# Performance work log

Hardware: AMD Instinct MI355X
Metric: run time of the kernel (lower is better)

## Reference

```python
import jax, jax.numpy as jnp
import numpy as np

P = 100   # num_proxies
N = 1024  # num_samples
D = 512


def _edge_index():
    # complete bipartite proxy<->sample graph, both directions, plus self-loops
    # (PyG GATConv adds self-loops for all nodes by default)
    p = np.arange(P)
    s = np.arange(P, P + N)
    src_ps = np.repeat(p, N)   # proxy -> sample
    dst_ps = np.tile(s, P)
    loops = np.arange(P + N)
    src = np.concatenate([src_ps, dst_ps, loops]).astype(np.int32)
    dst = np.concatenate([dst_ps, src_ps, loops]).astype(np.int32)
    return jnp.asarray(src), jnp.asarray(dst)


def setup_inputs() -> dict:
    key = jax.random.key(0)
    ks = jax.random.split(key, 10)
    sc = 1.0 / np.sqrt(D)
    src, dst = _edge_index()
    return {
        "x": jax.random.normal(ks[0], (N, D), jnp.float32),
        "proxies": jax.random.normal(ks[1], (P, D), jnp.float32),
        "W1": jax.random.normal(ks[2], (D, D), jnp.float32) * sc,
        "a_src1": jax.random.normal(ks[3], (D,), jnp.float32) * sc,
        "a_dst1": jax.random.normal(ks[4], (D,), jnp.float32) * sc,
        "b1": jnp.zeros((D,), jnp.float32),
        "W2": jax.random.normal(ks[5], (D, D), jnp.float32) * sc,
        "a_src2": jax.random.normal(ks[6], (D,), jnp.float32) * sc,
        "a_dst2": jax.random.normal(ks[7], (D,), jnp.float32) * sc,
        "b2": jnp.zeros((D,), jnp.float32),
        "fc_w": jax.random.normal(ks[8], (D, 100), jnp.float32) * sc,
        "fc_b": jnp.zeros((100,), jnp.float32),
        "src": src,
        "dst": dst,
    }


def _gat_conv(x, src, dst, W, a_src, a_dst, b, n_nodes):
    # PyG GATConv, heads=1, concat=True, negative_slope=0.2
    h = x @ W                      # [n, D]
    l_src = h @ a_src              # [n]
    l_dst = h @ a_dst              # [n]
    e = jax.nn.leaky_relu(l_src[src] + l_dst[dst], 0.2)   # [E]
    # segment softmax over edges sharing the same destination
    e = e - jax.ops.segment_max(e, dst, num_segments=n_nodes)[dst]
    ex = jnp.exp(e)
    denom = jax.ops.segment_sum(ex, dst, num_segments=n_nodes)[dst]
    alpha = ex / denom             # [E]
    out = jax.ops.segment_sum(alpha[:, None] * h[src], dst, num_segments=n_nodes)
    return out + b


def reference(x, proxies, W1, a_src1, a_dst1, b1, W2, a_src2, a_dst2, b2, fc_w, fc_b, src, dst):
    n = P + N
    h = jnp.concatenate([proxies, x], axis=0)          # [P+N, D]
    h = jax.nn.relu(_gat_conv(h, src, dst, W1, a_src1, a_dst1, b1, n))
    # Dropout -> identity (eval)
    h = jax.nn.relu(_gat_conv(h, src, dst, W2, a_src2, a_dst2, b2, n))
    preds = h @ fc_w + fc_b                            # [P+N, 100]
    return preds[P:], h[P:]
```

## Files before the change

### kernel.cpp

```cpp
#include <hip/hip_runtime.h>

#define PP 100
#define NS 1024
#define NN 1124
#define DD 512
#define CC 100
#define NTHR 256

typedef _Float16 f16;
typedef _Float16 f16x8 __attribute__((ext_vector_type(8)));
typedef float    f32x4 __attribute__((ext_vector_type(4)));

__device__ __forceinline__ float lk(float v) { return v > 0.f ? v : 0.2f * v; }
__device__ __forceinline__ f16 hif(float v) { return (f16)v; }
__device__ __forceinline__ f16 lof(float v) { return (f16)(v - (float)((f16)v)); }


__device__ __forceinline__ void mgemm_core(
    const f16* __restrict__ Ah, const f16* __restrict__ Al,
    const f16* __restrict__ Bth, const f16* __restrict__ Btl,
    int K, int row0, int col0, f16* __restrict__ lds, f32x4 acc[2][2])
{
  const int t = threadIdx.x;
  const int lane = t & 63, w = t >> 6;
  const int wr = w >> 1, wc = w & 1;
  const int srow = t >> 2, su = t & 3;
  const size_t aoff = (size_t)(row0 + srow) * K + su * 8;
  const size_t boff = (size_t)(col0 + srow) * K + su * 8;
  const int lw = srow * 40 + su * 8;
  const int fra = wr * 32 + (lane & 15);
  const int frb = wc * 32 + (lane & 15);
  const int fu  = (lane >> 4) * 8;
  f32x4 pa0 = *(const f32x4*)(Ah + aoff);
  f32x4 pa1 = *(const f32x4*)(Al + aoff);
  f32x4 pb0 = *(const f32x4*)(Bth + boff);
  f32x4 pb1 = *(const f32x4*)(Btl + boff);
  *(f32x4*)(lds + 0    + lw) = pa0;
  *(f32x4*)(lds + 2560 + lw) = pa1;
  *(f32x4*)(lds + 5120 + lw) = pb0;
  *(f32x4*)(lds + 7680 + lw) = pb1;
  if (K > 32) {
    pa0 = *(const f32x4*)(Ah + aoff + 32);
    pa1 = *(const f32x4*)(Al + aoff + 32);
    pb0 = *(const f32x4*)(Bth + boff + 32);
    pb1 = *(const f32x4*)(Btl + boff + 32);
  }
  __syncthreads();
  int cur = 0;
  for (int kt = 32; kt <= K; kt += 32) {
    f16* rb = lds + cur * 10240;
    f16* wb = lds + (cur ^ 1) * 10240;
    f16x8 ah[2], al[2], bh[2], bl[2];
#pragma unroll
    for (int m = 0; m < 2; ++m) {
      ah[m] = *(const f16x8*)(rb + (fra + m * 16) * 40 + fu);
      al[m] = *(const f16x8*)(rb + 2560 + (fra + m * 16) * 40 + fu);
    }
#pragma unroll
    for (int n = 0; n < 2; ++n) {
      bh[n] = *(const f16x8*)(rb + 5120 + (frb + n * 16) * 40 + fu);
      bl[n] = *(const f16x8*)(rb + 7680 + (frb + n * 16) * 40 + fu);
    }
    if (kt < K) {
      *(f32x4*)(wb + 0    + lw) = pa0;
      *(f32x4*)(wb + 2560 + lw) = pa1;
      *(f32x4*)(wb + 5120 + lw) = pb0;
      *(f32x4*)(wb + 7680 + lw) = pb1;
      if (kt + 32 < K) {
        pa0 = *(const f32x4*)(Ah + aoff + kt + 32);
        pa1 = *(const f32x4*)(Al + aoff + kt + 32);
        pb0 = *(const f32x4*)(Bth + boff + kt + 32);
        pb1 = *(const f32x4*)(Btl + boff + kt + 32);
      }
    }
#pragma unroll
    for (int m = 0; m < 2; ++m)
#pragma unroll
      for (int n = 0; n < 2; ++n) {
        acc[m][n] = __builtin_amdgcn_mfma_f32_16x16x32_f16(ah[m], bh[n], acc[m][n], 0, 0, 0);
        acc[m][n] = __builtin_amdgcn_mfma_f32_16x16x32_f16(al[m], bh[n], acc[m][n], 0, 0, 0);
        acc[m][n] = __builtin_amdgcn_mfma_f32_16x16x32_f16(ah[m], bl[n], acc[m][n], 0, 0, 0);
      }
    __syncthreads();
    cur ^= 1;
  }
}

__device__ __forceinline__ void agg_core(
    const float* __restrict__ lsrc, int kvalid,
    const float* __restrict__ ldb, const float* __restrict__ lsb,
    const f16* __restrict__ Bth, const f16* __restrict__ Btl,
    int K, int row0, int col0, int rvalid,
    const float* __restrict__ selfv,
    f16* __restrict__ outh, f16* __restrict__ outl,
    f16* __restrict__ lds, float* __restrict__ fred)
{
  const int t = threadIdx.x, lane = t & 63, w = t >> 6;
  const int wr = w >> 1, wc = w & 1;
  float* zred = fred;
  float* res  = fred + 256;
  float* riz  = fred + 320;
  const int srow = t >> 2, su = t & 3;
  float sm = -1e30f;
  for (int k = t; k < kvalid; k += NTHR) sm = fmaxf(sm, lsrc[k]);
#pragma unroll
  for (int off = 1; off < 64; off <<= 1) sm = fmaxf(sm, __shfl_xor(sm, off));
  if (lane == 0) zred[w] = sm;
  __syncthreads();
  sm = fmaxf(fmaxf(zred[0], zred[1]), fmaxf(zred[2], zred[3]));
  __syncthreads();
  const bool rok = (row0 + srow) < rvalid;
  float ldr = 0.f, mr = 0.f;
  if (rok) {
    ldr = ldb[row0 + srow];
    mr  = lk(fmaxf(sm, lsb[row0 + srow]) + ldr);
  }
  const size_t boff = (size_t)(col0 + srow) * K + su * 8;
  const int lw = srow * 40 + su * 8;
  const int fra = wr * 32 + (lane & 15);
  const int frb = wc * 32 + (lane & 15);
  const int fu  = (lane >> 4) * 8;
  f32x4 acc[2][2] = {};
  float zacc = 0.f;
  f32x4 pl0 = *(const f32x4*)(lsrc + su * 8);
  f32x4 pl1 = *(const f32x4*)(lsrc + su * 8 + 4);
  f32x4 pb0 = *(const f32x4*)(Bth + boff);
  f32x4 pb1 = *(const f32x4*)(Btl + boff);
  {
    f16x8 ae, al8;
#pragma unroll
    for (int j = 0; j < 8; ++j) {
      const int k = su * 8 + j;
      const float lv = (j < 4) ? pl0[j] : pl1[j - 4];
      float f = 0.f;
      if (rok && k < kvalid) f = __expf(lk(lv + ldr) - mr);
      zacc += f;
      ae[j] = hif(f); al8[j] = lof(f);
    }
    *(f16x8*)(lds + 0    + lw) = ae;
    *(f16x8*)(lds + 2560 + lw) = al8;
    *(f32x4*)(lds + 5120 + lw) = pb0;
    *(f32x4*)(lds + 7680 + lw) = pb1;
  }
  if (K > 32) {
    pl0 = *(const f32x4*)(lsrc + 32 + su * 8);
    pl1 = *(const f32x4*)(lsrc + 32 + su * 8 + 4);
    pb0 = *(const f32x4*)(Bth + boff + 32);
    pb1 = *(const f32x4*)(Btl + boff + 32);
  }
  __syncthreads();
  int cur = 0;
  for (int kt = 32; kt <= K; kt += 32) {
    f16* rb = lds + cur * 10240;
    f16* wb = lds + (cur ^ 1) * 10240;
    f16x8 ah[2], alr[2], bh[2], bl[2];
#pragma unroll
    for (int m = 0; m < 2; ++m) {
      ah[m]  = *(const f16x8*)(rb + (fra + m * 16) * 40 + fu);
      alr[m] = *(const f16x8*)(rb + 2560 + (fra + m * 16) * 40 + fu);
    }
#pragma unroll
    for (int n = 0; n < 2; ++n) {
      bh[n] = *(const f16x8*)(rb + 5120 + (frb + n * 16) * 40 + fu);
      bl[n] = *(const f16x8*)(rb + 7680 + (frb + n * 16) * 40 + fu);
    }
    if (kt < K) {
      f16x8 ae, al8;
      const int k0 = kt + su * 8;
#pragma unroll
      for (int j = 0; j < 8; ++j) {
        const int k = k0 + j;
        const float lv = (j < 4) ? pl0[j] : pl1[j - 4];
        float f = 0.f;
        if (rok && k < kvalid) f = __expf(lk(lv + ldr) - mr);
        zacc += f;
        ae[j] = hif(f); al8[j] = lof(f);
      }
      *(f16x8*)(wb + 0    + lw) = ae;
      *(f16x8*)(wb + 2560 + lw) = al8;
      *(f32x4*)(wb + 5120 + lw) = pb0;
      *(f32x4*)(wb + 7680 + lw) = pb1;
      if (kt + 32 < K) {
        pl0 = *(const f32x4*)(lsrc + kt + 32 + su * 8);
        pl1 = *(const f32x4*)(lsrc + kt + 32 + su * 8 + 4);
        pb0 = *(const f32x4*)(Bth + boff + kt + 32);
        pb1 = *(const f32x4*)(Btl + boff + kt + 32);
      }
    }
#pragma unroll
    for (int m = 0; m < 2; ++m)
#pragma unroll
      for (int n = 0; n < 2; ++n) {
        acc[m][n] = __builtin_amdgcn_mfma_f32_16x16x32_f16(ah[m],  bh[n], acc[m][n], 0, 0, 0);
        acc[m][n] = __builtin_amdgcn_mfma_f32_16x16x32_f16(alr[m], bh[n], acc[m][n], 0, 0, 0);
        acc[m][n] = __builtin_amdgcn_mfma_f32_16x16x32_f16(ah[m],  bl[n], acc[m][n], 0, 0, 0);
      }
    __syncthreads();
    cur ^= 1;
  }
  zred[t] = zacc;
  __syncthreads();
  if (t < 64) {
    float z = zred[t * 4] + zred[t * 4 + 1] + zred[t * 4 + 2] + zred[t * 4 + 3];
    float es = 0.f, iz = 0.f;
    if (row0 + t < rvalid) {
      const float l2 = ldb[row0 + t], s2 = lsb[row0 + t];
      const float m2 = lk(fmaxf(sm, s2) + l2);
      es = __expf(lk(s2 + l2) - m2);
      iz = 1.f / (z + es);
    }
    res[t] = es; riz[t] = iz;
  }
  __syncthreads();
#pragma unroll
  for (int m = 0; m < 2; ++m)
#pragma unroll
    for (int q = 0; q < 4; ++q) {
      const int rl = wr * 32 + m * 16 + (lane >> 4) * 4 + q;
      const int gr = row0 + rl;
      if (gr >= rvalid) continue;
      const float es = res[rl], iz = riz[rl];
#pragma unroll
      for (int n = 0; n < 2; ++n) {
        const int c = col0 + wc * 32 + n * 16 + (lane & 15);
        const float v = (acc[m][n][q] + es * selfv[(size_t)gr * DD + c]) * iz;
        outh[(size_t)gr * DD + c] = hif(v);
        outl[(size_t)gr * DD + c] = lof(v);
      }
    }
}

__device__ __forceinline__ void cvt_tile(
    const float* __restrict__ in, int R, int Cin,
    f16* __restrict__ oh, f16* __restrict__ ol, int ldo,
    int ti, int tj)
{
  const int t = threadIdx.x;
  const int gj0 = tj * 64 + (t & 31) * 2;
  const int i8  = (t >> 5) * 8;
  const bool c0 = gj0 < Cin, c1 = (gj0 + 1) < Cin;
  f16x8 vh0, vl0, vh1, vl1;
#pragma unroll
  for (int e = 0; e < 8; ++e) {
    const int gi = ti * 64 + i8 + e;
    float a = 0.f, b = 0.f;
    if (gi < R) {
      if (c0 && c1) {
        const float2 v = *(const float2*)(in + (size_t)gi * Cin + gj0);
        a = v.x; b = v.y;
      } else if (c0) {
        a = in[(size_t)gi * Cin + gj0];
      }
    }
    vh0[e] = hif(a); vl0[e] = lof(a);
    vh1[e] = hif(b); vl1[e] = lof(b);
  }
  const size_t o0 = (size_t)gj0 * ldo + ti * 64 + i8;
  *(f16x8*)(oh + o0) = vh0;
  *(f16x8*)(ol + o0) = vl0;
  const size_t o1 = o0 + ldo;
  *(f16x8*)(oh + o1) = vh1;
  *(f16x8*)(ol + o1) = vl1;
}

__global__ __launch_bounds__(NTHR) void prep1_k(
    const float* __restrict__ W1, const float* __restrict__ W2,
    const float* __restrict__ as1, const float* __restrict__ ad1,
    const float* __restrict__ as2, const float* __restrict__ ad2,
    float* __restrict__ v1s, float* __restrict__ v1d,
    float* __restrict__ v2s, float* __restrict__ v2d,
    float* __restrict__ ls2, float* __restrict__ ld2,
    float* __restrict__ M1pf, float* __restrict__ zP)
{
  const int u = blockIdx.x;
  if (u < 256) {
    const int wid  = u * 4 + (threadIdx.x >> 6);
    const int lane = threadIdx.x & 63;
    const int r = wid & 511;
    const bool l1 = (wid < 512);
    const float* W = l1 ? W1 : W2;
    const float4* a4 = (const float4*)(l1 ? as1 : as2);
    const float4* b4 = (const float4*)(l1 ? ad1 : ad2);
    const float4* w4 = (const float4*)(W + (size_t)r * DD);
    float4 w0 = w4[lane], w1 = w4[lane + 64];
    float4 a0 = a4[lane], a1 = a4[lane + 64];
    float4 b0 = b4[lane], b1 = b4[lane + 64];
    float s1 = w0.x * a0.x + w0.y * a0.y + w0.z * a0.z + w0.w * a0.w
             + w1.x * a1.x + w1.y * a1.y + w1.z * a1.z + w1.w * a1.w;
    float s2 = w0.x * b0.x + w0.y * b0.y + w0.z * b0.z + w0.w * b0.w
             + w1.x * b1.x + w1.y * b1.y + w1.z * b1.z + w1.w * b1.w;
#pragma unroll
    for (int off = 32; off > 0; off >>= 1) {
      s1 += __shfl_down(s1, off);
      s2 += __shfl_down(s2, off);
    }
    if (lane == 0) {
      (l1 ? v1s : v2s)[r] = s1;
      (l1 ? v1d : v2d)[r] = s2;
    }
  } else if (u == 256) {
    for (int i = threadIdx.x; i < 1152; i += NTHR) { ls2[i] = 0.f; ld2[i] = 0.f; }
    if (threadIdx.x < 128) zP[threadIdx.x] = 0.f;
  } else {
    float4* p4 = (float4*)M1pf + (size_t)(u - 257) * 800;
#pragma unroll
    for (int p = 0; p < 4; ++p) {
      const int i = threadIdx.x + p * 256;
      if (i < 800) p4[i] = make_float4(0.f, 0.f, 0.f, 0.f);
    }
  }
}

__global__ __launch_bounds__(NTHR) void prep2_k(
    const float* __restrict__ x, const float* __restrict__ prox,
    const float* __restrict__ W1, const float* __restrict__ W2,
    const float* __restrict__ fcw,
    const float* __restrict__ v1s, const float* __restrict__ v1d,
    f16* xth, f16* xtl, f16* pth, f16* ptl,
    f16* W1th, f16* W1tl, f16* W2th, f16* W2tl, f16* fwth, f16* fwtl,
    float* __restrict__ ls1, float* __restrict__ ld1)
{
  const int b = blockIdx.x;
  if (b < 64) {
    cvt_tile(W1, 512, 512, W1th, W1tl, 512, b >> 3, b & 7);
  } else if (b < 128) {
    cvt_tile(W2, 512, 512, W2th, W2tl, 512, (b - 64) >> 3, (b - 64) & 7);
  } else if (b < 256) {
    cvt_tile(x, NS, 512, xth, xtl, NS, (b - 128) >> 3, (b - 128) & 7);
  } else if (b < 272) {
    cvt_tile(prox, PP, 512, pth, ptl, 128, (b - 256) >> 3, (b - 256) & 7);
  } else if (b < 288) {
    cvt_tile(fcw, 512, CC, fwth, fwtl, 512, (b - 272) >> 1, (b - 272) & 1);
  } else {
    const int r    = (b - 288) * 4 + (threadIdx.x >> 6);
    const int lane = threadIdx.x & 63;
    if (r >= NN) return;
    const float* row = (r < PP) ? prox + (size_t)r * DD
                                : x + (size_t)(r - PP) * DD;
    const float4* r4 = (const float4*)row;
    const float4* s4 = (const float4*)v1s;
    const float4* d4 = (const float4*)v1d;
    float4 v0 = r4[lane], v1 = r4[lane + 64];
    float4 a0 = s4[lane], a1 = s4[lane + 64];
    float4 b0 = d4[lane], b1 = d4[lane + 64];
    float s1 = v0.x * a0.x + v0.y * a0.y + v0.z * a0.z + v0.w * a0.w
             + v1.x * a1.x + v1.y * a1.y + v1.z * a1.z + v1.w * a1.w;
    float s2 = v0.x * b0.x + v0.y * b0.y + v0.z * b0.z + v0.w * b0.w
             + v1.x * b1.x + v1.y * b1.y + v1.z * b1.z + v1.w * b1.w;
#pragma unroll
    for (int off = 32; off > 0; off >>= 1) {
      s1 += __shfl_down(s1, off);
      s2 += __shfl_down(s2, off);
    }
    if (lane == 0) { ls1[r] = s1; ld1[r] = s2; }
  }
}

__global__ __launch_bounds__(NTHR) void agg1x_k(
    const float* __restrict__ ls1, const float* __restrict__ ld1,
    const f16* __restrict__ pth, const f16* __restrict__ ptl,
    const f16* __restrict__ xth, const f16* __restrict__ xtl,
    const float* __restrict__ x,
    float* __restrict__ M1pf, float* __restrict__ zP,
    f16* __restrict__ M1h, f16* __restrict__ M1l)
{
  __shared__ __align__(16) f16 lds[20480];
  __shared__ float fred[384];
  const int b = blockIdx.x;
  if (b < 128) {
    const int row0 = (b >> 3) * 64, col0 = (b & 7) * 64;
    agg_core(ls1, PP, ld1 + PP, ls1 + PP, pth, ptl, 128, row0, col0, NS,
             x, M1h + (size_t)PP * DD, M1l + (size_t)PP * DD, lds, fred);
    return;
  }
  const int t = threadIdx.x, lane = t & 63, w = t >> 6;
  const int wr = w >> 1, wc = w & 1;
  const int b2 = b - 128;
  const int tile = b2 >> 2, chunk = b2 & 3;
  const int row0 = (tile >> 3) * 64, col0 = (tile & 7) * 64;
  const int k0 = chunk * 256;
  const float* lsrc = ls1 + PP;
  float sm = -1e30f;
  for (int k = t; k < NS; k += NTHR) sm = fmaxf(sm, lsrc[k]);
#pragma unroll
  for (int off = 1; off < 64; off <<= 1) sm = fmaxf(sm, __shfl_xor(sm, off));
  if (lane == 0) fred[w] = sm;
  __syncthreads();
  sm = fmaxf(fmaxf(fred[0], fred[1]), fmaxf(fred[2], fred[3]));
  __syncthreads();
  const int srow = t >> 2, su = t & 3;
  const bool rok = (row0 + srow) < PP;
  float ldr = 0.f, mr = 0.f;
  if (rok) {
    ldr = ld1[row0 + srow];
    mr  = lk(fmaxf(sm, ls1[row0 + srow]) + ldr);
  }
  const size_t boff = (size_t)(col0 + srow) * NS + k0 + su * 8;
  const int lw = srow * 40 + su * 8;
  const int fra = wr * 32 + (lane & 15);
  const int frb = wc * 32 + (lane & 15);
  const int fu  = (lane >> 4) * 8;
  f32x4 acc[2][2] = {};
  float zacc = 0.f;
  f32x4 pl0 = *(const f32x4*)(lsrc + k0 + su * 8);
  f32x4 pl1 = *(const f32x4*)(lsrc + k0 + su * 8 + 4);
  f32x4 pb0 = *(const f32x4*)(xth + boff);
  f32x4 pb1 = *(const f32x4*)(xtl + boff);
  {
    f16x8 ae, al8;
#pragma unroll
    for (int j = 0; j < 8; ++j) {
      const float lv = (j < 4) ? pl0[j] : pl1[j - 4];
      float f = 0.f;
      if (rok) f = __expf(lk(lv + ldr) - mr);
      zacc += f;
      ae[j] = hif(f); al8[j] = lof(f);
    }
    *(f16x8*)(lds + 0    + lw) = ae;
    *(f16x8*)(lds + 2560 + lw) = al8;
    *(f32x4*)(lds + 5120 + lw) = pb0;
    *(f32x4*)(lds + 7680 + lw) = pb1;
  }
  pl0 = *(const f32x4*)(lsrc + k0 + 32 + su * 8);
  pl1 = *(const f32x4*)(lsrc + k0 + 32 + su * 8 + 4);
  pb0 = *(const f32x4*)(xth + boff + 32);
  pb1 = *(const f32x4*)(xtl + boff + 32);
  __syncthreads();
  int cur = 0;
  for (int kt = 32; kt <= 256; kt += 32) {
    f16* rb = lds + cur * 10240;
    f16* wb = lds + (cur ^ 1) * 10240;
    f16x8 ah[2], alr[2], bh[2], bl[2];
#pragma unroll
    for (int m = 0; m < 2; ++m) {
      ah[m]  = *(const f16x8*)(rb + (fra + m * 16) * 40 + fu);
      alr[m] = *(const f16x8*)(rb + 2560 + (fra + m * 16) * 40 + fu);
    }
#pragma unroll
    for (int n = 0; n < 2; ++n) {
      bh[n] = *(const f16x8*)(rb + 5120 + (frb + n * 16) * 40 + fu);
      bl[n] = *(const f16x8*)(rb + 7680 + (frb + n * 16) * 40 + fu);
    }
    if (kt < 256) {
      f16x8 ae, al8;
#pragma unroll
      for (int j = 0; j < 8; ++j) {
        const float lv = (j < 4) ? pl0[j] : pl1[j - 4];
        float f = 0.f;
        if (rok) f = __expf(lk(lv + ldr) - mr);
        zacc += f;
        ae[j] = hif(f); al8[j] = lof(f);
      }
      *(f16x8*)(wb + 0    + lw) = ae;
      *(f16x8*)(wb + 2560 + lw) = al8;
      *(f32x4*)(wb + 5120 + lw) = pb0;
      *(f32x4*)(wb + 7680 + lw) = pb1;
      if (kt + 32 < 256) {
        pl0 = *(const f32x4*)(lsrc + k0 + kt + 32 + su * 8);
        pl1 = *(const f32x4*)(lsrc + k0 + kt + 32 + su * 8 + 4);
        pb0 = *(const f32x4*)(xth + boff + kt + 32);
        pb1 = *(const f32x4*)(xtl + boff + kt + 32);
      }
    }
#pragma unroll
    for (int m = 0; m < 2; ++m)
#pragma unroll
      for (int n = 0; n < 2; ++n) {
        acc[m][n] = __builtin_amdgcn_mfma_f32_16x16x32_f16(ah[m],  bh[n], acc[m][n], 0, 0, 0);
        acc[m][n] = __builtin_amdgcn_mfma_f32_16x16x32_f16(alr[m], bh[n], acc[m][n], 0, 0, 0);
        acc[m][n] = __builtin_amdgcn_mfma_f32_16x16x32_f16(ah[m],  bl[n], acc[m][n], 0, 0, 0);
      }
    __syncthreads();
    cur ^= 1;
  }
  if (col0 == 0) {
    fred[t] = zacc;
    __syncthreads();
    if (t < 64) {
      const int r = row0 + t;
      if (r < PP) {
        float z = fred[t * 4] + fred[t * 4 + 1] + fred[t * 4 + 2] + fred[t * 4 + 3];
        atomicAdd(&zP[r], z);
      }
    }
  }
#pragma unroll
  for (int m = 0; m < 2; ++m)
#pragma unroll
    for (int q = 0; q < 4; ++q) {
      const int gr = row0 + wr * 32 + m * 16 + (lane >> 4) * 4 + q;
      if (gr >= PP) continue;
#pragma unroll
      for (int n = 0; n < 2; ++n) {
        const int c = col0 + wc * 32 + n * 16 + (lane & 15);
        atomicAdd(&M1pf[(size_t)gr * DD + c], acc[m][n][q]);
      }
    }
}

__global__ __launch_bounds__(NTHR) void h1_k(
    const f16* __restrict__ M1h, const f16* __restrict__ M1l,
    const float* __restrict__ M1pf, const float* __restrict__ zP,
    const float* __restrict__ ls1, const float* __restrict__ ld1,
    const float* __restrict__ prox,
    const f16* __restrict__ W1th, const f16* __restrict__ W1tl,
    const float* __restrict__ b1,
    const float* __restrict__ v2s, const float* __restrict__ v2d,
    float* __restrict__ h1, f16* __restrict__ h1pth, f16* __restrict__ h1ptl,
    float* __restrict__ ls2, float* __restrict__ ld2)
{
  __shared__ __align__(16) f16 lds[20480];
  __shared__ float fred[384];
  float* esA = fred + 256;
  float* izA = fred + 320;
  const int t = threadIdx.x, lane = t & 63, w = t >> 6, wr = w >> 1, wc = w & 1;
  const int b = blockIdx.x;
  const int row0 = (b >> 3) * 64, col0 = (b & 7) * 64;
  const bool hasP = (row0 < 128);
  if (hasP) {
    float sm = -1e30f;
    for (int k = t; k < NS; k += NTHR) sm = fmaxf(sm, ls1[PP + k]);
#pragma unroll
    for (int off = 1; off < 64; off <<= 1) sm = fmaxf(sm, __shfl_xor(sm, off));
    if (lane == 0) fred[w] = sm;
    __syncthreads();
    sm = fmaxf(fmaxf(fred[0], fred[1]), fmaxf(fred[2], fred[3]));
    if (t < 64) {
      const int r = row0 + t;
      float es = 0.f, iz = 0.f;
      if (r < PP) {
        const float ldr = ld1[r];
        const float m = lk(fmaxf(sm, ls1[r]) + ldr);
        es = __expf(lk(ls1[r] + ldr) - m);
        iz = 1.f / (zP[r] + es);
      }
      esA[t] = es; izA[t] = iz;
    }
    __syncthreads();
  }
  const int srow = t >> 2, su = t & 3;
  const int ar = row0 + srow;
  const bool isP = ar < PP;
  const size_t aoff = (size_t)ar * DD + su * 8;
  const size_t boff = (size_t)(col0 + srow) * DD + su * 8;
  const int lw = srow * 40 + su * 8;
  const int fra = wr * 32 + (lane & 15);
  const int frb = wc * 32 + (lane & 15);
  const int fu  = (lane >> 4) * 8;
  const float esr = isP ? esA[srow] : 0.f;
  const float izr = isP ? izA[srow] : 0.f;
  f32x4 qa0, qa1, qb0, qb1, pb0, pb1;
  auto loadA = [&](int k) {
    if (isP) {
      qa0 = *(const f32x4*)(M1pf + aoff + k);
      qa1 = *(const f32x4*)(M1pf + aoff + k + 4);
      qb0 = *(const f32x4*)(prox + aoff + k);
      qb1 = *(const f32x4*)(prox + aoff + k + 4);
    } else {
      qa0 = *(const f32x4*)(M1h + aoff + k);
      qa1 = *(const f32x4*)(M1l + aoff + k);
    }
  };
  auto storeA = [&](f16* wb) {
    if (isP) {
      f16x8 hh, ll;
#pragma unroll
      for (int j = 0; j < 8; ++j) {
        const float pv = (j < 4) ? qa0[j] : qa1[j - 4];
        const float xv = (j < 4) ? qb0[j] : qb1[j - 4];
        const float v = (pv + esr * xv) * izr;
        hh[j] = hif(v); ll[j] = lof(v);
      }
      *(f16x8*)(wb + lw) = hh;
      *(f16x8*)(wb + 2560 + lw) = ll;
    } else {
      *(f32x4*)(wb + lw) = qa0;
      *(f32x4*)(wb + 2560 + lw) = qa1;
    }
  };
  f32x4 acc[2][2] = {};
  loadA(0);
  pb0 = *(const f32x4*)(W1th + boff);
  pb1 = *(const f32x4*)(W1tl + boff);
  storeA(lds);
  *(f32x4*)(lds + 5120 + lw) = pb0;
  *(f32x4*)(lds + 7680 + lw) = pb1;
  loadA(32);
  pb0 = *(const f32x4*)(W1th + boff + 32);
  pb1 = *(const f32x4*)(W1tl + boff + 32);
  __syncthreads();
  int cur = 0;
  for (int kt = 32; kt <= DD; kt += 32) {
    f16* rb = lds + cur * 10240;
    f16* wb = lds + (cur ^ 1) * 10240;
    f16x8 ah[2], al[2], bh[2], bl[2];
#pragma unroll
    for (int m = 0; m < 2; ++m) {
      ah[m] = *(const f16x8*)(rb + (fra + m * 16) * 40 + fu);
      al[m] = *(const f16x8*)(rb + 2560 + (fra + m * 16) * 40 + fu);
    }
#pragma unroll
    for (int n = 0; n < 2; ++n) {
      bh[n] = *(const f16x8*)(rb + 5120 + (frb + n * 16) * 40 + fu);
      bl[n] = *(const f16x8*)(rb + 7680 + (frb + n * 16) * 40 + fu);
    }
    if (kt < DD) {
      storeA(wb);
      *(f32x4*)(wb + 5120 + lw) = pb0;
      *(f32x4*)(wb + 7680 + lw) = pb1;
      if (kt + 32 < DD) {
        loadA(kt + 32);
        pb0 = *(const f32x4*)(W1th + boff + kt + 32);
        pb1 = *(const f32x4*)(W1tl + boff + kt + 32);
      }
    }
#pragma unroll
    for (int m = 0; m < 2; ++m)
#pragma unroll
      for (int n = 0; n < 2; ++n) {
        acc[m][n] = __builtin_amdgcn_mfma_f32_16x16x32_f16(ah[m], bh[n], acc[m][n], 0, 0, 0);
        acc[m][n] = __builtin_amdgcn_mfma_f32_16x16x32_f16(al[m], bh[n], acc[m][n], 0, 0, 0);
        acc[m][n] = __builtin_amdgcn_mfma_f32_16x16x32_f16(ah[m], bl[n], acc[m][n], 0, 0, 0);
      }
    __syncthreads();
    cur ^= 1;
  }
  const int c0 = col0 + wc * 32 + (lane & 15);
  const int c1 = c0 + 16;
  const float vs0 = v2s[c0], vs1 = v2s[c1];
  const float vd0 = v2d[c0], vd1 = v2d[c1];
  const float bb0 = b1[c0],  bb1 = b1[c1];
#pragma unroll
  for (int m = 0; m < 2; ++m)
#pragma unroll
    for (int q = 0; q < 4; ++q) {
      const int r = row0 + wr * 32 + m * 16 + (lane >> 4) * 4 + q;
      if (r >= NN) continue;
      float ps = 0.f, pd = 0.f;
#pragma unroll
      for (int n = 0; n < 2; ++n) {
        const int c = (n == 0) ? c0 : c1;
        const float v = fmaxf(acc[m][n][q] + (n == 0 ? bb0 : bb1), 0.f);
        h1[(size_t)r * DD + c] = v;
        ps += v * (n == 0 ? vs0 : vs1);
        pd += v * (n == 0 ? vd0 : vd1);
        if (r < 128) {
          const size_t o = (size_t)c * 128 + r;
          f16 hh = (f16)0.f, ll = (f16)0.f;
          if (r < PP) { hh = hif(v); ll = lof(v); }
          h1pth[o] = hh; h1ptl[o] = ll;
        }
      }
#pragma unroll
      for (int off = 1; off < 16; off <<= 1) {
        ps += __shfl_xor(ps, off);
        pd += __shfl_xor(pd, off);
      }
      if ((lane & 15) == 0) {
        atomicAdd(&ls2[r], ps);
        atomicAdd(&ld2[r], pd);
      }
    }
}

__global__ __launch_bounds__(NTHR) void agg2x_k(
    const float* __restrict__ ls2, const float* __restrict__ ld2,
    const f16* __restrict__ h1pth, const f16* __restrict__ h1ptl,
    const float* __restrict__ h1,
    f16* __restrict__ M2h, f16* __restrict__ M2l)
{
  __shared__ __align__(16) f16 lds[20480];
  __shared__ float fred[384];
  const int b = blockIdx.x;
  const int row0 = (b >> 3) * 64, col0 = (b & 7) * 64;
  agg_core(ls2, PP, ld2 + PP, ls2 + PP, h1pth, h1ptl, 128, row0, col0, NS,
           h1 + (size_t)PP * DD, M2h, M2l, lds, fred);
}

__global__ __launch_bounds__(NTHR) void h2_k(
    const f16* __restrict__ M2h, const f16* __restrict__ M2l,
    const f16* __restrict__ W2th, const f16* __restrict__ W2tl,
    const float* __restrict__ b2, float* __restrict__ h2s,
    f16* __restrict__ h2h, f16* __restrict__ h2l)
{
  __shared__ __align__(16) f16 lds[20480];
  f32x4 acc[2][2] = {};
  const int t = threadIdx.x, lane = t & 63, w = t >> 6, wr = w >> 1, wc = w & 1;
  const int b = blockIdx.x;
  const int row0 = (b >> 3) * 64, col0 = (b & 7) * 64;
  mgemm_core(M2h, M2l, W2th, W2tl, DD, row0, col0, lds, acc);
#pragma unroll
  for (int m = 0; m < 2; ++m)
#pragma unroll
    for (int q = 0; q < 4; ++q) {
      const int r = row0 + wr * 32 + m * 16 + (lane >> 4) * 4 + q;
#pragma unroll
      for (int n = 0; n < 2; ++n) {
        const int c = col0 + wc * 32 + n * 16 + (lane & 15);
        const float v = fmaxf(acc[m][n][q] + b2[c], 0.f);
        const size_t o = (size_t)r * DD + c;
        h2s[o] = v;
        h2h[o] = hif(v); h2l[o] = lof(v);
      }
    }
}

__global__ __launch_bounds__(NTHR) void fc_k(
    const f16* __restrict__ h2h, const f16* __restrict__ h2l,
    const f16* __restrict__ fwth, const f16* __restrict__ fwtl,
    const float* __restrict__ fcb, float* __restrict__ out)
{
  __shared__ __align__(16) f16 lds[20480];
  f32x4 acc[2][2] = {};
  const int t = threadIdx.x, lane = t & 63, w = t >> 6, wr = w >> 1, wc = w & 1;
  const int b = blockIdx.x;
  const int row0 = (b >> 1) * 64, col0 = (b & 1) * 64;
  mgemm_core(h2h, h2l, fwth, fwtl, DD, row0, col0, lds, acc);
#pragma unroll
  for (int m = 0; m < 2; ++m)
#pragma unroll
    for (int q = 0; q < 4; ++q) {
      const int r = row0 + wr * 32 + m * 16 + (lane >> 4) * 4 + q;
#pragma unroll
      for (int n = 0; n < 2; ++n) {
        const int c = col0 + wc * 32 + n * 16 + (lane & 15);
        if (c < CC) out[(size_t)r * CC + c] = acc[m][n][q] + fcb[c];
      }
    }
}

extern "C" void kernel_launch(void* const* d_in, const int* in_sizes, int n_in,
                              void* d_out, int out_size, void* d_ws, size_t ws_size,
                              hipStream_t stream)
{
  const float* x    = (const float*)d_in[0];
  const float* prox = (const float*)d_in[1];
  const float* W1   = (const float*)d_in[2];
  const float* as1  = (const float*)d_in[3];
  const float* ad1  = (const float*)d_in[4];
  const float* b1   = (const float*)d_in[5];
  const float* W2   = (const float*)d_in[6];
  const float* as2  = (const float*)d_in[7];
  const float* ad2  = (const float*)d_in[8];
  const float* b2   = (const float*)d_in[9];
  const float* fcw  = (const float*)d_in[10];
  const float* fcb  = (const float*)d_in[11];
  float* out = (float*)d_out;

  float* F = (float*)d_ws;
  float* h1   = F; F += (size_t)NN * DD;
  float* ls1  = F; F += 1152;
  float* ld1  = F; F += 1152;
  float* ls2  = F; F += 1152;
  float* ld2  = F; F += 1152;
  float* v1s  = F; F += DD;
  float* v1d  = F; F += DD;
  float* v2s  = F; F += DD;
  float* v2d  = F; F += DD;
  float* M1pf = F; F += (size_t)128 * DD;
  float* zP   = F; F += 128;
  f16* H = (f16*)F;
  f16* M1h  = H; H += (size_t)1152 * DD;
  f16* M1l  = H; H += (size_t)1152 * DD;
  f16* M2h  = H; H += (size_t)NS * DD;
  f16* M2l  = H; H += (size_t)NS * DD;
  f16* xth  = H; H += (size_t)DD * NS;
  f16* xtl  = H; H += (size_t)DD * NS;
  f16* pth  = H; H += (size_t)DD * 128;
  f16* ptl  = H; H += (size_t)DD * 128;
  f16* W1th = H; H += (size_t)DD * DD;
  f16* W1tl = H; H += (size_t)DD * DD;
  f16* W2th = H; H += (size_t)DD * DD;
  f16* W2tl = H; H += (size_t)DD * DD;
  f16* fwth = H; H += (size_t)128 * DD;
  f16* fwtl = H; H += (size_t)128 * DD;
  f16* h2h  = H; H += (size_t)NS * DD;
  f16* h2l  = H; H += (size_t)NS * DD;
  f16* h1pth = H; H += (size_t)DD * 128;
  f16* h1ptl = H; H += (size_t)DD * 128;
  float* h2s = out + (size_t)NS * CC;

  dim3 blk(NTHR);
  prep1_k<<<dim3(273), blk, 0, stream>>>(W1, W2, as1, ad1, as2, ad2,
                                         v1s, v1d, v2s, v2d, ls2, ld2,
                                         M1pf, zP);
  prep2_k<<<dim3(569), blk, 0, stream>>>(x, prox, W1, W2, fcw, v1s, v1d,
      xth, xtl, pth, ptl, W1th, W1tl, W2th, W2tl, fwth, fwtl, ls1, ld1);
  agg1x_k<<<dim3(192), blk, 0, stream>>>(ls1, ld1, pth, ptl, xth, xtl,
                                         x, M1pf, zP, M1h, M1l);
  h1_k<<<dim3(144), blk, 0, stream>>>(M1h, M1l, M1pf, zP, ls1, ld1, prox,
                                      W1th, W1tl, b1, v2s, v2d,
                                      h1, h1pth, h1ptl, ls2, ld2);
  agg2x_k<<<dim3(128), blk, 0, stream>>>(ls2, ld2, h1pth, h1ptl, h1, M2h, M2l);
  h2_k<<<dim3(128), blk, 0, stream>>>(M2h, M2l, W2th, W2tl, b2, h2s, h2h, h2l);
  fc_k<<<dim3(32), blk, 0, stream>>>(h2h, h2l, fwth, fwtl, fcb, out);
}
```

Before: 141.9 us.

## Double threads per GEMM block with split A/B loaders and smaller per-wave tiles

Raises GEMM-style kernels from 256 to 512 threads (8 waves), each wave computing a 16x32 subtile instead of 32x32. Loading is split so the first half of the threads stage A (including softmax weight computation) and the second half stage B. This is meant to raise per-block wave parallelism and latency hiding for these small-grid kernels. In exchange each wave reuses its fragments less and issues more LDS fragment reads per MFMA, and the larger blocks may lower occupancy.

```diff
diff --git a/kernel.cpp b/kernel.cpp
--- a/kernel.cpp
+++ b/kernel.cpp
@@ -6,6 +6,7 @@
 #define DD 512
 #define CC 100
 #define NTHR 256
+#define GT  512
 
 typedef _Float16 f16;
 typedef _Float16 f16x8 __attribute__((ext_vector_type(8)));
@@ -15,72 +16,61 @@
 __device__ __forceinline__ f16 hif(float v) { return (f16)v; }
 __device__ __forceinline__ f16 lof(float v) { return (f16)(v - (float)((f16)v)); }
 
+#define MFMA16(a, b, c) __builtin_amdgcn_mfma_f32_16x16x32_f16(a, b, c, 0, 0, 0)
+
 
 __device__ __forceinline__ void mgemm_core(
     const f16* __restrict__ Ah, const f16* __restrict__ Al,
     const f16* __restrict__ Bth, const f16* __restrict__ Btl,
-    int K, int row0, int col0, f16* __restrict__ lds, f32x4 acc[2][2])
+    int K, int row0, int col0, f16* __restrict__ lds, f32x4 acc[2])
 {
   const int t = threadIdx.x;
   const int lane = t & 63, w = t >> 6;
   const int wr = w >> 1, wc = w & 1;
-  const int srow = t >> 2, su = t & 3;
-  const size_t aoff = (size_t)(row0 + srow) * K + su * 8;
-  const size_t boff = (size_t)(col0 + srow) * K + su * 8;
+  const bool isA = t < 256;
+  const int tt = t & 255;
+  const int srow = tt >> 2, su = tt & 3;
   const int lw = srow * 40 + su * 8;
-  const int fra = wr * 32 + (lane & 15);
+  const int sec0 = isA ? 0 : 5120, sec1 = isA ? 2560 : 7680;
+  const f16* g0 = isA ? Ah : Bth;
+  const f16* g1 = isA ? Al : Btl;
+  const size_t goff = (size_t)((isA ? row0 : col0) + srow) * K + su * 8;
+  const int fra = wr * 16 + (lane & 15);
   const int frb = wc * 32 + (lane & 15);
   const int fu  = (lane >> 4) * 8;
-  f32x4 pa0 = *(const f32x4*)(Ah + aoff);
-  f32x4 pa1 = *(const f32x4*)(Al + aoff);
-  f32x4 pb0 = *(const f32x4*)(Bth + boff);
-  f32x4 pb1 = *(const f32x4*)(Btl + boff);
-  *(f32x4*)(lds + 0    + lw) = pa0;
-  *(f32x4*)(lds + 2560 + lw) = pa1;
-  *(f32x4*)(lds + 5120 + lw) = pb0;
-  *(f32x4*)(lds + 7680 + lw) = pb1;
+  f32x4 p0 = *(const f32x4*)(g0 + goff);
+  f32x4 p1 = *(const f32x4*)(g1 + goff);
+  *(f32x4*)(lds + sec0 + lw) = p0;
+  *(f32x4*)(lds + sec1 + lw) = p1;
   if (K > 32) {
-    pa0 = *(const f32x4*)(Ah + aoff + 32);
-    pa1 = *(const f32x4*)(Al + aoff + 32);
-    pb0 = *(const f32x4*)(Bth + boff + 32);
-    pb1 = *(const f32x4*)(Btl + boff + 32);
+    p0 = *(const f32x4*)(g0 + goff + 32);
+    p1 = *(const f32x4*)(g1 + goff + 32);
   }
   __syncthreads();
   int cur = 0;
   for (int kt = 32; kt <= K; kt += 32) {
     f16* rb = lds + cur * 10240;
     f16* wb = lds + (cur ^ 1) * 10240;
-    f16x8 ah[2], al[2], bh[2], bl[2];
-#pragma unroll
-    for (int m = 0; m < 2; ++m) {
-      ah[m] = *(const f16x8*)(rb + (fra + m * 16) * 40 + fu);
-      al[m] = *(const f16x8*)(rb + 2560 + (fra + m * 16) * 40 + fu);
-    }
-#pragma unroll
-    for (int n = 0; n < 2; ++n) {
-      bh[n] = *(const f16x8*)(rb + 5120 + (frb + n * 16) * 40 + fu);
-      bl[n] = *(const f16x8*)(rb + 7680 + (frb + n * 16) * 40 + fu);
-    }
+    f16x8 ah  = *(const f16x8*)(rb + fra * 40 + fu);
+    f16x8 al  = *(const f16x8*)(rb + 2560 + fra * 40 + fu);
+    f16x8 bh0 = *(const f16x8*)(rb + 5120 + frb * 40 + fu);
+    f16x8 bl0 = *(const f16x8*)(rb + 7680 + frb * 40 + fu);
+    f16x8 bh1 = *(const f16x8*)(rb + 5120 + (frb + 16) * 40 + fu);
+    f16x8 bl1 = *(const f16x8*)(rb + 7680 + (frb + 16) * 40 + fu);
     if (kt < K) {
-      *(f32x4*)(wb + 0    + lw) = pa0;
-      *(f32x4*)(wb + 2560 + lw) = pa1;
-      *(f32x4*)(wb + 5120 + lw) = pb0;
-      *(f32x4*)(wb + 7680 + lw) = pb1;
+      *(f32x4*)(wb + sec0 + lw) = p0;
+      *(f32x4*)(wb + sec1 + lw) = p1;
       if (kt + 32 < K) {
-        pa0 = *(const f32x4*)(Ah + aoff + kt + 32);
-        pa1 = *(const f32x4*)(Al + aoff + kt + 32);
-        pb0 = *(const f32x4*)(Bth + boff + kt + 32);
-        pb1 = *(const f32x4*)(Btl + boff + kt + 32);
-      }
-    }
-#pragma unroll
-    for (int m = 0; m < 2; ++m)
-#pragma unroll
-      for (int n = 0; n < 2; ++n) {
-        acc[m][n] = __builtin_amdgcn_mfma_f32_16x16x32_f16(ah[m], bh[n], acc[m][n], 0, 0, 0);
-        acc[m][n] = __builtin_amdgcn_mfma_f32_16x16x32_f16(al[m], bh[n], acc[m][n], 0, 0, 0);
-        acc[m][n] = __builtin_amdgcn_mfma_f32_16x16x32_f16(ah[m], bl[n], acc[m][n], 0, 0, 0);
-      }
+        p0 = *(const f32x4*)(g0 + goff + kt + 32);
+        p1 = *(const f32x4*)(g1 + goff + kt + 32);
+      }
+    }
+    acc[0] = MFMA16(ah, bh0, acc[0]);
+    acc[0] = MFMA16(al, bh0, acc[0]);
+    acc[0] = MFMA16(ah, bl0, acc[0]);
+    acc[1] = MFMA16(ah, bh1, acc[1]);
+    acc[1] = MFMA16(al, bh1, acc[1]);
+    acc[1] = MFMA16(ah, bl1, acc[1]);
     __syncthreads();
     cur ^= 1;
   }
@@ -100,105 +90,94 @@
   float* zred = fred;
   float* res  = fred + 256;
   float* riz  = fred + 320;
-  const int srow = t >> 2, su = t & 3;
   float sm = -1e30f;
-  for (int k = t; k < kvalid; k += NTHR) sm = fmaxf(sm, lsrc[k]);
+  for (int k = t; k < kvalid; k += GT) sm = fmaxf(sm, lsrc[k]);
 #pragma unroll
   for (int off = 1; off < 64; off <<= 1) sm = fmaxf(sm, __shfl_xor(sm, off));
   if (lane == 0) zred[w] = sm;
   __syncthreads();
-  sm = fmaxf(fmaxf(zred[0], zred[1]), fmaxf(zred[2], zred[3]));
-  __syncthreads();
-  const bool rok = (row0 + srow) < rvalid;
-  float ldr = 0.f, mr = 0.f;
-  if (rok) {
+  sm = fmaxf(fmaxf(fmaxf(zred[0], zred[1]), fmaxf(zred[2], zred[3])),
+             fmaxf(fmaxf(zred[4], zred[5]), fmaxf(zred[6], zred[7])));
+  __syncthreads();
+  const bool isA = t < 256;
+  const int tt = t & 255;
+  const int srow = tt >> 2, su = tt & 3;
+  const int lw = srow * 40 + su * 8;
+  bool rok = false; float ldr = 0.f, mr = 0.f;
+  if (isA && (row0 + srow) < rvalid) {
+    rok = true;
     ldr = ldb[row0 + srow];
     mr  = lk(fmaxf(sm, lsb[row0 + srow]) + ldr);
   }
   const size_t boff = (size_t)(col0 + srow) * K + su * 8;
-  const int lw = srow * 40 + su * 8;
-  const int fra = wr * 32 + (lane & 15);
+  const int fra = wr * 16 + (lane & 15);
   const int frb = wc * 32 + (lane & 15);
   const int fu  = (lane >> 4) * 8;
-  f32x4 acc[2][2] = {};
+  f32x4 acc[2] = {};
   float zacc = 0.f;
-  f32x4 pl0 = *(const f32x4*)(lsrc + su * 8);
-  f32x4 pl1 = *(const f32x4*)(lsrc + su * 8 + 4);
-  f32x4 pb0 = *(const f32x4*)(Bth + boff);
-  f32x4 pb1 = *(const f32x4*)(Btl + boff);
-  {
-    f16x8 ae, al8;
-#pragma unroll
-    for (int j = 0; j < 8; ++j) {
-      const int k = su * 8 + j;
-      const float lv = (j < 4) ? pl0[j] : pl1[j - 4];
-      float f = 0.f;
-      if (rok && k < kvalid) f = __expf(lk(lv + ldr) - mr);
-      zacc += f;
-      ae[j] = hif(f); al8[j] = lof(f);
-    }
-    *(f16x8*)(lds + 0    + lw) = ae;
-    *(f16x8*)(lds + 2560 + lw) = al8;
-    *(f32x4*)(lds + 5120 + lw) = pb0;
-    *(f32x4*)(lds + 7680 + lw) = pb1;
-  }
-  if (K > 32) {
-    pl0 = *(const f32x4*)(lsrc + 32 + su * 8);
-    pl1 = *(const f32x4*)(lsrc + 32 + su * 8 + 4);
-    pb0 = *(const f32x4*)(Bth + boff + 32);
-    pb1 = *(const f32x4*)(Btl + boff + 32);
-  }
+  f32x4 p0, p1;
+  if (isA) {
+    p0 = *(const f32x4*)(lsrc + su * 8);
+    p1 = *(const f32x4*)(lsrc + su * 8 + 4);
+  } else {
+    p0 = *(const f32x4*)(Bth + boff);
+    p1 = *(const f32x4*)(Btl + boff);
+  }
+  auto stage = [&](f16* buf, int kbase) {
+    if (isA) {
+      f16x8 ae, al8;
+#pragma unroll
+      for (int j = 0; j < 8; ++j) {
+        const int k = kbase + su * 8 + j;
+        const float lv = (j < 4) ? p0[j] : p1[j - 4];
+        float f = 0.f;
+        if (rok && k < kvalid) f = __expf(lk(lv + ldr) - mr);
+        zacc += f;
+        ae[j] = hif(f); al8[j] = lof(f);
+      }
+      *(f16x8*)(buf + lw) = ae;
+      *(f16x8*)(buf + 2560 + lw) = al8;
+    } else {
+      *(f32x4*)(buf + 5120 + lw) = p0;
+      *(f32x4*)(buf + 7680 + lw) = p1;
+    }
+  };
+  auto prefetch = [&](int k) {
+    if (isA) {
+      p0 = *(const f32x4*)(lsrc + k + su * 8);
+      p1 = *(const f32x4*)(lsrc + k + su * 8 + 4);
+    } else {
+      p0 = *(const f32x4*)(Bth + boff + k);
+      p1 = *(const f32x4*)(Btl + boff + k);
+    }
+  };
+  stage(lds, 0);
+  if (K > 32) prefetch(32);
   __syncthreads();
   int cur = 0;
   for (int kt = 32; kt <= K; kt += 32) {
     f16* rb = lds + cur * 10240;
     f16* wb = lds + (cur ^ 1) * 10240;
-    f16x8 ah[2], alr[2], bh[2], bl[2];
-#pragma unroll
-    for (int m = 0; m < 2; ++m) {
-      ah[m]  = *(const f16x8*)(rb + (fra + m * 16) * 40 + fu);
-      alr[m] = *(const f16x8*)(rb + 2560 + (fra + m * 16) * 40 + fu);
-    }
-#pragma unroll
-    for (int n = 0; n < 2; ++n) {
-      bh[n] = *(const f16x8*)(rb + 5120 + (frb + n * 16) * 40 + fu);
-      bl[n] = *(const f16x8*)(rb + 7680 + (frb + n * 16) * 40 + fu);
-    }
+    f16x8 ah  = *(const f16x8*)(rb + fra * 40 + fu);
+    f16x8 al  = *(const f16x8*)(rb + 2560 + fra * 40 + fu);
+    f16x8 bh0 = *(const f16x8*)(rb + 5120 + frb * 40 + fu);
+    f16x8 bl0 = *(const f16x8*)(rb + 7680 + frb * 40 + fu);
+    f16x8 bh1 = *(const f16x8*)(rb + 5120 + (frb + 16) * 40 + fu);
+    f16x8 bl1 = *(const f16x8*)(rb + 7680 + (frb + 16) * 40 + fu);
     if (kt < K) {
-      f16x8 ae, al8;
-      const int k0 = kt + su * 8;
-#pragma unroll
-      for (int j = 0; j < 8; ++j) {
-        const int k = k0 + j;
-        const float lv = (j < 4) ? pl0[j] : pl1[j - 4];
-        float f = 0.f;
-        if (rok && k < kvalid) f = __expf(lk(lv + ldr) - mr);
-        zacc += f;
-        ae[j] = hif(f); al8[j] = lof(f);
-      }
-      *(f16x8*)(wb + 0    + lw) = ae;
-      *(f16x8*)(wb + 2560 + lw) = al8;
-      *(f32x4*)(wb + 5120 + lw) = pb0;
-      *(f32x4*)(wb + 7680 + lw) = pb1;
-      if (kt + 32 < K) {
-        pl0 = *(const f32x4*)(lsrc + kt + 32 + su * 8);
-        pl1 = *(const f32x4*)(lsrc + kt + 32 + su * 8 + 4);
-        pb0 = *(const f32x4*)(Bth + boff + kt + 32);
-        pb1 = *(const f32x4*)(Btl + boff + kt + 32);
-      }
-    }
-#pragma unroll
-    for (int m = 0; m < 2; ++m)
-#pragma unroll
-      for (int n = 0; n < 2; ++n) {
-        acc[m][n] = __builtin_amdgcn_mfma_f32_16x16x32_f16(ah[m],  bh[n], acc[m][n], 0, 0, 0);
-        acc[m][n] = __builtin_amdgcn_mfma_f32_16x16x32_f16(alr[m], bh[n], acc[m][n], 0, 0, 0);
-        acc[m][n] = __builtin_amdgcn_mfma_f32_16x16x32_f16(ah[m],  bl[n], acc[m][n], 0, 0, 0);
-      }
+      stage(wb, kt);
+      if (kt + 32 < K) prefetch(kt + 32);
+    }
+    acc[0] = MFMA16(ah, bh0, acc[0]);
+    acc[0] = MFMA16(al, bh0, acc[0]);
+    acc[0] = MFMA16(ah, bl0, acc[0]);
+    acc[1] = MFMA16(ah, bh1, acc[1]);
+    acc[1] = MFMA16(al, bh1, acc[1]);
+    acc[1] = MFMA16(ah, bl1, acc[1]);
     __syncthreads();
     cur ^= 1;
   }
-  zred[t] = zacc;
+  if (t < 256) zred[t] = zacc;
   __syncthreads();
   if (t < 64) {
     float z = zred[t * 4] + zred[t * 4 + 1] + zred[t * 4 + 2] + zred[t * 4 + 3];
@@ -213,21 +192,19 @@
   }
   __syncthreads();
 #pragma unroll
-  for (int m = 0; m < 2; ++m)
-#pragma unroll
-    for (int q = 0; q < 4; ++q) {
-      const int rl = wr * 32 + m * 16 + (lane >> 4) * 4 + q;
-      const int gr = row0 + rl;
-      if (gr >= rvalid) continue;
-      const float es = res[rl], iz = riz[rl];
-#pragma unroll
-      for (int n = 0; n < 2; ++n) {
-        const int c = col0 + wc * 32 + n * 16 + (lane & 15);
-        const float v = (acc[m][n][q] + es * selfv[(size_t)gr * DD + c]) * iz;
-        outh[(size_t)gr * DD + c] = hif(v);
-        outl[(size_t)gr * DD + c] = lof(v);
-      }
-    }
+  for (int q = 0; q < 4; ++q) {
+    const int rl = wr * 16 + (lane >> 4) * 4 + q;
+    const int gr = row0 + rl;
+    if (gr >= rvalid) continue;
+    const float es = res[rl], iz = riz[rl];
+#pragma unroll
+    for (int n = 0; n < 2; ++n) {
+      const int c = col0 + wc * 32 + n * 16 + (lane & 15);
+      const float v = (acc[n][q] + es * selfv[(size_t)gr * DD + c]) * iz;
+      outh[(size_t)gr * DD + c] = hif(v);
+      outl[(size_t)gr * DD + c] = lof(v);
+    }
+  }
 }
 
 __device__ __forceinline__ void cvt_tile(
@@ -356,7 +333,7 @@
   }
 }
 
-__global__ __launch_bounds__(NTHR) void agg1x_k(
+__global__ __launch_bounds__(GT) void agg1x_k(
     const float* __restrict__ ls1, const float* __restrict__ ld1,
     const f16* __restrict__ pth, const f16* __restrict__ ptl,
     const f16* __restrict__ xth, const f16* __restrict__ xtl,
@@ -381,100 +358,87 @@
   const int k0 = chunk * 256;
   const float* lsrc = ls1 + PP;
   float sm = -1e30f;
-  for (int k = t; k < NS; k += NTHR) sm = fmaxf(sm, lsrc[k]);
+  for (int k = t; k < NS; k += GT) sm = fmaxf(sm, lsrc[k]);
 #pragma unroll
   for (int off = 1; off < 64; off <<= 1) sm = fmaxf(sm, __shfl_xor(sm, off));
   if (lane == 0) fred[w] = sm;
   __syncthreads();
-  sm = fmaxf(fmaxf(fred[0], fred[1]), fmaxf(fred[2], fred[3]));
-  __syncthreads();
-  const int srow = t >> 2, su = t & 3;
-  const bool rok = (row0 + srow) < PP;
-  float ldr = 0.f, mr = 0.f;
-  if (rok) {
+  sm = fmaxf(fmaxf(fmaxf(fred[0], fred[1]), fmaxf(fred[2], fred[3])),
+             fmaxf(fmaxf(fred[4], fred[5]), fmaxf(fred[6], fred[7])));
+  __syncthreads();
+  const bool isA = t < 256;
+  const int tt = t & 255;
+  const int srow = tt >> 2, su = tt & 3;
+  const int lw = srow * 40 + su * 8;
+  bool rok = false; float ldr = 0.f, mr = 0.f;
+  if (isA && (row0 + srow) < PP) {
+    rok = true;
     ldr = ld1[row0 + srow];
     mr  = lk(fmaxf(sm, ls1[row0 + srow]) + ldr);
   }
   const size_t boff = (size_t)(col0 + srow) * NS + k0 + su * 8;
-  const int lw = srow * 40 + su * 8;
-  const int fra = wr * 32 + (lane & 15);
+  const int fra = wr * 16 + (lane & 15);
   const int frb = wc * 32 + (lane & 15);
   const int fu  = (lane >> 4) * 8;
-  f32x4 acc[2][2] = {};
+  f32x4 acc[2] = {};
   float zacc = 0.f;
-  f32x4 pl0 = *(const f32x4*)(lsrc + k0 + su * 8);
-  f32x4 pl1 = *(const f32x4*)(lsrc + k0 + su * 8 + 4);
-  f32x4 pb0 = *(const f32x4*)(xth + boff);
-  f32x4 pb1 = *(const f32x4*)(xtl + boff);
-  {
-    f16x8 ae, al8;
-#pragma unroll
-    for (int j = 0; j < 8; ++j) {
-      const float lv = (j < 4) ? pl0[j] : pl1[j - 4];
-      float f = 0.f;
-      if (rok) f = __expf(lk(lv + ldr) - mr);
-      zacc += f;
-      ae[j] = hif(f); al8[j] = lof(f);
-    }
-    *(f16x8*)(lds + 0    + lw) = ae;
-    *(f16x8*)(lds + 2560 + lw) = al8;
-    *(f32x4*)(lds + 5120 + lw) = pb0;
-    *(f32x4*)(lds + 7680 + lw) = pb1;
-  }
-  pl0 = *(const f32x4*)(lsrc + k0 + 32 + su * 8);
-  pl1 = *(const f32x4*)(lsrc + k0 + 32 + su * 8 + 4);
-  pb0 = *(const f32x4*)(xth + boff + 32);
-  pb1 = *(const f32x4*)(xtl + boff + 32);
+  f32x4 p0, p1;
+  auto prefetch = [&](int k) {
+    if (isA) {
+      p0 = *(const f32x4*)(lsrc + k0 + k + su * 8);
+      p1 = *(const f32x4*)(lsrc + k0 + k + su * 8 + 4);
+    } else {
+      p0 = *(const f32x4*)(xth + boff + k);
+      p1 = *(const f32x4*)(xtl + boff + k);
+    }
+  };
+  auto stage = [&](f16* buf) {
+    if (isA) {
+      f16x8 ae, al8;
+#pragma unroll
+      for (int j = 0; j < 8; ++j) {
+        const float lv = (j < 4) ? p0[j] : p1[j - 4];
+        float f = 0.f;
+        if (rok) f = __expf(lk(lv + ldr) - mr);
+        zacc += f;
+        ae[j] = hif(f); al8[j] = lof(f);
+      }
+      *(f16x8*)(buf + lw) = ae;
+      *(f16x8*)(buf + 2560 + lw) = al8;
+    } else {
+      *(f32x4*)(buf + 5120 + lw) = p0;
+      *(f32x4*)(buf + 7680 + lw) = p1;
+    }
+  };
+  prefetch(0);
+  stage(lds);
+  prefetch(32);
   __syncthreads();
   int cur = 0;
   for (int kt = 32; kt <= 256; kt += 32) {
     f16* rb = lds + cur * 10240;
     f16* wb = lds + (cur ^ 1) * 10240;
-    f16x8 ah[2], alr[2], bh[2], bl[2];
-#pragma unroll
-    for (int m = 0; m < 2; ++m) {
-      ah[m]  = *(const f16x8*)(rb + (fra + m * 16) * 40 + fu);
-      alr[m] = *(const f16x8*)(rb + 2560 + (fra + m * 16) * 40 + fu);
-    }
-#pragma unroll
-    for (int n = 0; n < 2; ++n) {
-      bh[n] = *(const f16x8*)(rb + 5120 + (frb + n * 16) * 40 + fu);
-      bl[n] = *(const f16x8*)(rb + 7680 + (frb + n * 16) * 40 + fu);
-    }
+    f16x8 ah  = *(const f16x8*)(rb + fra * 40 + fu);
+    f16x8 al  = *(const f16x8*)(rb + 2560 + fra * 40 + fu);
+    f16x8 bh0 = *(const f16x8*)(rb + 5120 + frb * 40 + fu);
+    f16x8 bl0 = *(const f16x8*)(rb + 7680 + frb * 40 + fu);
+    f16x8 bh1 = *(const f16x8*)(rb + 5120 + (frb + 16) * 40 + fu);
+    f16x8 bl1 = *(const f16x8*)(rb + 7680 + (frb + 16) * 40 + fu);
     if (kt < 256) {
-      f16x8 ae, al8;
-#pragma unroll
-      for (int j = 0; j < 8; ++j) {
-        const float lv = (j < 4) ? pl0[j] : pl1[j - 4];
-        float f = 0.f;
-        if (rok) f = __expf(lk(lv + ldr) - mr);
-        zacc += f;
-        ae[j] = hif(f); al8[j] = lof(f);
-      }
-      *(f16x8*)(wb + 0    + lw) = ae;
-      *(f16x8*)(wb + 2560 + lw) = al8;
-      *(f32x4*)(wb + 5120 + lw) = pb0;
-      *(f32x4*)(wb + 7680 + lw) = pb1;
-      if (kt + 32 < 256) {
-        pl0 = *(const f32x4*)(lsrc + k0 + kt + 32 + su * 8);
-        pl1 = *(const f32x4*)(lsrc + k0 + kt + 32 + su * 8 + 4);
-        pb0 = *(const f32x4*)(xth + boff + kt + 32);
-        pb1 = *(const f32x4*)(xtl + boff + kt + 32);
-      }
-    }
-#pragma unroll
-    for (int m = 0; m < 2; ++m)
-#pragma unroll
-      for (int n = 0; n < 2; ++n) {
-        acc[m][n] = __builtin_amdgcn_mfma_f32_16x16x32_f16(ah[m],  bh[n], acc[m][n], 0, 0, 0);
-        acc[m][n] = __builtin_amdgcn_mfma_f32_16x16x32_f16(alr[m], bh[n], acc[m][n], 0, 0, 0);
-        acc[m][n] = __builtin_amdgcn_mfma_f32_16x16x32_f16(ah[m],  bl[n], acc[m][n], 0, 0, 0);
-      }
+      stage(wb);
+      if (kt + 32 < 256) prefetch(kt + 32);
+    }
+    acc[0] = MFMA16(ah, bh0, acc[0]);
+    acc[0] = MFMA16(al, bh0, acc[0]);
+    acc[0] = MFMA16(ah, bl0, acc[0]);
+    acc[1] = MFMA16(ah, bh1, acc[1]);
+    acc[1] = MFMA16(al, bh1, acc[1]);
+    acc[1] = MFMA16(ah, bl1, acc[1]);
     __syncthreads();
     cur ^= 1;
   }
   if (col0 == 0) {
-    fred[t] = zacc;
+    if (t < 256) fred[t] = zacc;
     __syncthreads();
     if (t < 64) {
       const int r = row0 + t;
@@ -485,20 +449,18 @@
     }
   }
 #pragma unroll
-  for (int m = 0; m < 2; ++m)
-#pragma unroll
-    for (int q = 0; q < 4; ++q) {
-      const int gr = row0 + wr * 32 + m * 16 + (lane >> 4) * 4 + q;
-      if (gr >= PP) continue;
-#pragma unroll
-      for (int n = 0; n < 2; ++n) {
-        const int c = col0 + wc * 32 + n * 16 + (lane & 15);
-        atomicAdd(&M1pf[(size_t)gr * DD + c], acc[m][n][q]);
-      }
-    }
-}
-
-__global__ __launch_bounds__(NTHR) void h1_k(
+  for (int q = 0; q < 4; ++q) {
+    const int gr = row0 + wr * 16 + (lane >> 4) * 4 + q;
+    if (gr >= PP) continue;
+#pragma unroll
+    for (int n = 0; n < 2; ++n) {
+      const int c = col0 + wc * 32 + n * 16 + (lane & 15);
+      atomicAdd(&M1pf[(size_t)gr * DD + c], acc[n][q]);
+    }
+  }
+}
+
+__global__ __launch_bounds__(GT) void h1_k(
     const f16* __restrict__ M1h, const f16* __restrict__ M1l,
     const float* __restrict__ M1pf, const float* __restrict__ zP,
     const float* __restrict__ ls1, const float* __restrict__ ld1,
@@ -513,18 +475,20 @@
   __shared__ float fred[384];
   float* esA = fred + 256;
   float* izA = fred + 320;
-  const int t = threadIdx.x, lane = t & 63, w = t >> 6, wr = w >> 1, wc = w & 1;
+  const int t = threadIdx.x, lane = t & 63, w = t >> 6;
+  const int wr = w >> 1, wc = w & 1;
   const int b = blockIdx.x;
   const int row0 = (b >> 3) * 64, col0 = (b & 7) * 64;
   const bool hasP = (row0 < 128);
   if (hasP) {
     float sm = -1e30f;
-    for (int k = t; k < NS; k += NTHR) sm = fmaxf(sm, ls1[PP + k]);
+    for (int k = t; k < NS; k += GT) sm = fmaxf(sm, ls1[PP + k]);
 #pragma unroll
     for (int off = 1; off < 64; off <<= 1) sm = fmaxf(sm, __shfl_xor(sm, off));
     if (lane == 0) fred[w] = sm;
     __syncthreads();
-    sm = fmaxf(fmaxf(fred[0], fred[1]), fmaxf(fred[2], fred[3]));
+    sm = fmaxf(fmaxf(fmaxf(fred[0], fred[1]), fmaxf(fred[2], fred[3])),
+               fmaxf(fmaxf(fred[4], fred[5]), fmaxf(fred[6], fred[7])));
     if (t < 64) {
       const int r = row0 + t;
       float es = 0.f, iz = 0.f;
@@ -538,90 +502,83 @@
     }
     __syncthreads();
   }
-  const int srow = t >> 2, su = t & 3;
+  const bool isA = t < 256;
+  const int tt = t & 255;
+  const int srow = tt >> 2, su = tt & 3;
+  const int lw = srow * 40 + su * 8;
   const int ar = row0 + srow;
-  const bool isP = ar < PP;
+  const bool isP = isA && (ar < PP);
   const size_t aoff = (size_t)ar * DD + su * 8;
   const size_t boff = (size_t)(col0 + srow) * DD + su * 8;
-  const int lw = srow * 40 + su * 8;
-  const int fra = wr * 32 + (lane & 15);
+  const int fra = wr * 16 + (lane & 15);
   const int frb = wc * 32 + (lane & 15);
   const int fu  = (lane >> 4) * 8;
   const float esr = isP ? esA[srow] : 0.f;
   const float izr = isP ? izA[srow] : 0.f;
-  f32x4 qa0, qa1, qb0, qb1, pb0, pb1;
-  auto loadA = [&](int k) {
-    if (isP) {
-      qa0 = *(const f32x4*)(M1pf + aoff + k);
-      qa1 = *(const f32x4*)(M1pf + aoff + k + 4);
-      qb0 = *(const f32x4*)(prox + aoff + k);
-      qb1 = *(const f32x4*)(prox + aoff + k + 4);
+  f32x4 qa0, qa1, qb0, qb1;
+  auto loadS = [&](int k) {
+    if (isA) {
+      if (isP) {
+        qa0 = *(const f32x4*)(M1pf + aoff + k);
+        qa1 = *(const f32x4*)(M1pf + aoff + k + 4);
+        qb0 = *(const f32x4*)(prox + aoff + k);
+        qb1 = *(const f32x4*)(prox + aoff + k + 4);
+      } else {
+        qa0 = *(const f32x4*)(M1h + aoff + k);
+        qa1 = *(const f32x4*)(M1l + aoff + k);
+      }
     } else {
-      qa0 = *(const f32x4*)(M1h + aoff + k);
-      qa1 = *(const f32x4*)(M1l + aoff + k);
+      qa0 = *(const f32x4*)(W1th + boff + k);
+      qa1 = *(const f32x4*)(W1tl + boff + k);
     }
   };
-  auto storeA = [&](f16* wb) {
-    if (isP) {
-      f16x8 hh, ll;
-#pragma unroll
-      for (int j = 0; j < 8; ++j) {
-        const float pv = (j < 4) ? qa0[j] : qa1[j - 4];
-        const float xv = (j < 4) ? qb0[j] : qb1[j - 4];
-        const float v = (pv + esr * xv) * izr;
-        hh[j] = hif(v); ll[j] = lof(v);
-      }
-      *(f16x8*)(wb + lw) = hh;
-      *(f16x8*)(wb + 2560 + lw) = ll;
+  auto storeS = [&](f16* wb) {
+    if (isA) {
+      if (isP) {
+        f16x8 hh, ll;
+#pragma unroll
+        for (int j = 0; j < 8; ++j) {
+          const float pv = (j < 4) ? qa0[j] : qa1[j - 4];
+          const float xv = (j < 4) ? qb0[j] : qb1[j - 4];
+          const float v = (pv + esr * xv) * izr;
+          hh[j] = hif(v); ll[j] = lof(v);
+        }
+        *(f16x8*)(wb + lw) = hh;
+        *(f16x8*)(wb + 2560 + lw) = ll;
+      } else {
+        *(f32x4*)(wb + lw) = qa0;
+        *(f32x4*)(wb + 2560 + lw) = qa1;
+      }
     } else {
-      *(f32x4*)(wb + lw) = qa0;
-      *(f32x4*)(wb + 2560 + lw) = qa1;
+      *(f32x4*)(wb + 5120 + lw) = qa0;
+      *(f32x4*)(wb + 7680 + lw) = qa1;
     }
   };
-  f32x4 acc[2][2] = {};
-  loadA(0);
-  pb0 = *(const f32x4*)(W1th + boff);
-  pb1 = *(const f32x4*)(W1tl + boff);
-  storeA(lds);
-  *(f32x4*)(lds + 5120 + lw) = pb0;
-  *(f32x4*)(lds + 7680 + lw) = pb1;
-  loadA(32);
-  pb0 = *(const f32x4*)(W1th + boff + 32);
-  pb1 = *(const f32x4*)(W1tl + boff + 32);
+  f32x4 acc[2] = {};
+  loadS(0);
+  storeS(lds);
+  loadS(32);
   __syncthreads();
   int cur = 0;
   for (int kt = 32; kt <= DD; kt += 32) {
     f16* rb = lds + cur * 10240;
     f16* wb = lds + (cur ^ 1) * 10240;
-    f16x8 ah[2], al[2], bh[2], bl[2];
-#pragma unroll
-    for (int m = 0; m < 2; ++m) {
-      ah[m] = *(const f16x8*)(rb + (fra + m * 16) * 40 + fu);
-      al[m] = *(const f16x8*)(rb + 2560 + (fra + m * 16) * 40 + fu);
-    }
-#pragma unroll
-    for (int n = 0; n < 2; ++n) {
-      bh[n] = *(const f16x8*)(rb + 5120 + (frb + n * 16) * 40 + fu);
-      bl[n] = *(const f16x8*)(rb + 7680 + (frb + n * 16) * 40 + fu);
-    }
+    f16x8 ah  = *(const f16x8*)(rb + fra * 40 + fu);
+    f16x8 al  = *(const f16x8*)(rb + 2560 + fra * 40 + fu);
+    f16x8 bh0 = *(const f16x8*)(rb + 5120 + frb * 40 + fu);
+    f16x8 bl0 = *(const f16x8*)(rb + 7680 + frb * 40 + fu);
+    f16x8 bh1 = *(const f16x8*)(rb + 5120 + (frb + 16) * 40 + fu);
+    f16x8 bl1 = *(const f16x8*)(rb + 7680 + (frb + 16) * 40 + fu);
     if (kt < DD) {
-      storeA(wb);
-      *(f32x4*)(wb + 5120 + lw) = pb0;
-      *(f32x4*)(wb + 7680 + lw) = pb1;
-      if (kt + 32 < DD) {
-        loadA(kt + 32);
-        pb0 = *(const f32x4*)(W1th + boff + kt + 32);
-        pb1 = *(const f32x4*)(W1tl + boff + kt + 32);
-      }
-    }
-#pragma unroll
-    for (int m = 0; m < 2; ++m)
-#pragma unroll
-      for (int n = 0; n < 2; ++n) {
-        acc[m][n] = __builtin_amdgcn_mfma_f32_16x16x32_f16(ah[m], bh[n], acc[m][n], 0, 0, 0);
-        acc[m][n] = __builtin_amdgcn_mfma_f32_16x16x32_f16(al[m], bh[n], acc[m][n], 0, 0, 0);
-        acc[m][n] = __builtin_amdgcn_mfma_f32_16x16x32_f16(ah[m], bl[n], acc[m][n], 0, 0, 0);
-      }
+      storeS(wb);
+      if (kt + 32 < DD) loadS(kt + 32);
+    }
+    acc[0] = MFMA16(ah, bh0, acc[0]);
+    acc[0] = MFMA16(al, bh0, acc[0]);
+    acc[0] = MFMA16(ah, bl0, acc[0]);
+    acc[1] = MFMA16(ah, bh1, acc[1]);
+    acc[1] = MFMA16(al, bh1, acc[1]);
+    acc[1] = MFMA16(ah, bl1, acc[1]);
     __syncthreads();
     cur ^= 1;
   }
@@ -631,39 +588,37 @@
   const float vd0 = v2d[c0], vd1 = v2d[c1];
   const float bb0 = b1[c0],  bb1 = b1[c1];
 #pragma unroll
-  for (int m = 0; m < 2; ++m)
-#pragma unroll
-    for (int q = 0; q < 4; ++q) {
-      const int r = row0 + wr * 32 + m * 16 + (lane >> 4) * 4 + q;
-      if (r >= NN) continue;
-      float ps = 0.f, pd = 0.f;
-#pragma unroll
-      for (int n = 0; n < 2; ++n) {
-        const int c = (n == 0) ? c0 : c1;
-        const float v = fmaxf(acc[m][n][q] + (n == 0 ? bb0 : bb1), 0.f);
-        h1[(size_t)r * DD + c] = v;
-        ps += v * (n == 0 ? vs0 : vs1);
-        pd += v * (n == 0 ? vd0 : vd1);
-        if (r < 128) {
-          const size_t o = (size_t)c * 128 + r;
-          f16 hh = (f16)0.f, ll = (f16)0.f;
-          if (r < PP) { hh = hif(v); ll = lof(v); }
-          h1pth[o] = hh; h1ptl[o] = ll;
-        }
-      }
-#pragma unroll
-      for (int off = 1; off < 16; off <<= 1) {
-        ps += __shfl_xor(ps, off);
-        pd += __shfl_xor(pd, off);
-      }
-      if ((lane & 15) == 0) {
-        atomicAdd(&ls2[r], ps);
-        atomicAdd(&ld2[r], pd);
-      }
-    }
-}
-
-__global__ __launch_bounds__(NTHR) void agg2x_k(
+  for (int q = 0; q < 4; ++q) {
+    const int r = row0 + wr * 16 + (lane >> 4) * 4 + q;
+    if (r >= NN) continue;
+    float ps = 0.f, pd = 0.f;
+#pragma unroll
+    for (int n = 0; n < 2; ++n) {
+      const int c = (n == 0) ? c0 : c1;
+      const float v = fmaxf(acc[n][q] + (n == 0 ? bb0 : bb1), 0.f);
+      h1[(size_t)r * DD + c] = v;
+      ps += v * (n == 0 ? vs0 : vs1);
+      pd += v * (n == 0 ? vd0 : vd1);
+      if (r < 128) {
+        const size_t o = (size_t)c * 128 + r;
+        f16 hh = (f16)0.f, ll = (f16)0.f;
+        if (r < PP) { hh = hif(v); ll = lof(v); }
+        h1pth[o] = hh; h1ptl[o] = ll;
+      }
+    }
+#pragma unroll
+    for (int off = 1; off < 16; off <<= 1) {
+      ps += __shfl_xor(ps, off);
+      pd += __shfl_xor(pd, off);
+    }
+    if ((lane & 15) == 0) {
+      atomicAdd(&ls2[r], ps);
+      atomicAdd(&ld2[r], pd);
+    }
+  }
+}
+
+__global__ __launch_bounds__(GT) void agg2x_k(
     const float* __restrict__ ls2, const float* __restrict__ ld2,
     const f16* __restrict__ h1pth, const f16* __restrict__ h1ptl,
     const float* __restrict__ h1,
@@ -677,56 +632,54 @@
            h1 + (size_t)PP * DD, M2h, M2l, lds, fred);
 }
 
-__global__ __launch_bounds__(NTHR) void h2_k(
+__global__ __launch_bounds__(GT) void h2_k(
     const f16* __restrict__ M2h, const f16* __restrict__ M2l,
     const f16* __restrict__ W2th, const f16* __restrict__ W2tl,
     const float* __restrict__ b2, float* __restrict__ h2s,
     f16* __restrict__ h2h, f16* __restrict__ h2l)
 {
   __shared__ __align__(16) f16 lds[20480];
-  f32x4 acc[2][2] = {};
-  const int t = threadIdx.x, lane = t & 63, w = t >> 6, wr = w >> 1, wc = w & 1;
+  f32x4 acc[2] = {};
+  const int t = threadIdx.x, lane = t & 63, w = t >> 6;
+  const int wr = w >> 1, wc = w & 1;
   const int b = blockIdx.x;
   const int row0 = (b >> 3) * 64, col0 = (b & 7) * 64;
   mgemm_core(M2h, M2l, W2th, W2tl, DD, row0, col0, lds, acc);
 #pragma unroll
-  for (int m = 0; m < 2; ++m)
-#pragma unroll
-    for (int q = 0; q < 4; ++q) {
-      const int r = row0 + wr * 32 + m * 16 + (lane >> 4) * 4 + q;
-#pragma unroll
-      for (int n = 0; n < 2; ++n) {
-        const int c = col0 + wc * 32 + n * 16 + (lane & 15);
-        const float v = fmaxf(acc[m][n][q] + b2[c], 0.f);
-        const size_t o = (size_t)r * DD + c;
-        h2s[o] = v;
-        h2h[o] = hif(v); h2l[o] = lof(v);
-      }
-    }
-}
-
-__global__ __launch_bounds__(NTHR) void fc_k(
+  for (int q = 0; q < 4; ++q) {
+    const int r = row0 + wr * 16 + (lane >> 4) * 4 + q;
+#pragma unroll
+    for (int n = 0; n < 2; ++n) {
+      const int c = col0 + wc * 32 + n * 16 + (lane & 15);
+      const float v = fmaxf(acc[n][q] + b2[c], 0.f);
+      const size_t o = (size_t)r * DD + c;
+      h2s[o] = v;
+      h2h[o] = hif(v); h2l[o] = lof(v);
+    }
+  }
+}
+
+__global__ __launch_bounds__(GT) void fc_k(
     const f16* __restrict__ h2h, const f16* __restrict__ h2l,
     const f16* __restrict__ fwth, const f16* __restrict__ fwtl,
     const float* __restrict__ fcb, float* __restrict__ out)
 {
   __shared__ __align__(16) f16 lds[20480];
-  f32x4 acc[2][2] = {};
-  const int t = threadIdx.x, lane = t & 63, w = t >> 6, wr = w >> 1, wc = w & 1;
+  f32x4 acc[2] = {};
+  const int t = threadIdx.x, lane = t & 63, w = t >> 6;
+  const int wr = w >> 1, wc = w & 1;
   const int b = blockIdx.x;
   const int row0 = (b >> 1) * 64, col0 = (b & 1) * 64;
   mgemm_core(h2h, h2l, fwth, fwtl, DD, row0, col0, lds, acc);
 #pragma unroll
-  for (int m = 0; m < 2; ++m)
-#pragma unroll
-    for (int q = 0; q < 4; ++q) {
-      const int r = row0 + wr * 32 + m * 16 + (lane >> 4) * 4 + q;
-#pragma unroll
-      for (int n = 0; n < 2; ++n) {
-        const int c = col0 + wc * 32 + n * 16 + (lane & 15);
-        if (c < CC) out[(size_t)r * CC + c] = acc[m][n][q] + fcb[c];
-      }
-    }
+  for (int q = 0; q < 4; ++q) {
+    const int r = row0 + wr * 16 + (lane >> 4) * 4 + q;
+#pragma unroll
+    for (int n = 0; n < 2; ++n) {
+      const int c = col0 + wc * 32 + n * 16 + (lane & 15);
+      if (c < CC) out[(size_t)r * CC + c] = acc[n][q] + fcb[c];
+    }
+  }
 }
 
 extern "C" void kernel_launch(void* const* d_in, const int* in_sizes, int n_in,
@@ -780,18 +733,19 @@
   f16* h1ptl = H; H += (size_t)DD * 128;
   float* h2s = out + (size_t)NS * CC;
 
-  dim3 blk(NTHR);
-  prep1_k<<<dim3(273), blk, 0, stream>>>(W1, W2, as1, ad1, as2, ad2,
-                                         v1s, v1d, v2s, v2d, ls2, ld2,
-                                         M1pf, zP);
-  prep2_k<<<dim3(569), blk, 0, stream>>>(x, prox, W1, W2, fcw, v1s, v1d,
+  prep1_k<<<dim3(273), dim3(NTHR), 0, stream>>>(W1, W2, as1, ad1, as2, ad2,
+                                                v1s, v1d, v2s, v2d, ls2, ld2,
+                                                M1pf, zP);
+  prep2_k<<<dim3(569), dim3(NTHR), 0, stream>>>(x, prox, W1, W2, fcw, v1s, v1d,
       xth, xtl, pth, ptl, W1th, W1tl, W2th, W2tl, fwth, fwtl, ls1, ld1);
-  agg1x_k<<<dim3(192), blk, 0, stream>>>(ls1, ld1, pth, ptl, xth, xtl,
-                                         x, M1pf, zP, M1h, M1l);
-  h1_k<<<dim3(144), blk, 0, stream>>>(M1h, M1l, M1pf, zP, ls1, ld1, prox,
-                                      W1th, W1tl, b1, v2s, v2d,
-                                      h1, h1pth, h1ptl, ls2, ld2);
-  agg2x_k<<<dim3(128), blk, 0, stream>>>(ls2, ld2, h1pth, h1ptl, h1, M2h, M2l);
-  h2_k<<<dim3(128), blk, 0, stream>>>(M2h, M2l, W2th, W2tl, b2, h2s, h2h, h2l);
-  fc_k<<<dim3(32), blk, 0, stream>>>(h2h, h2l, fwth, fwtl, fcb, out);
-}
+  agg1x_k<<<dim3(192), dim3(GT), 0, stream>>>(ls1, ld1, pth, ptl, xth, xtl,
+                                              x, M1pf, zP, M1h, M1l);
+  h1_k<<<dim3(144), dim3(GT), 0, stream>>>(M1h, M1l, M1pf, zP, ls1, ld1, prox,
+                                           W1th, W1tl, b1, v2s, v2d,
+                                           h1, h1pth, h1ptl, ls2, ld2);
+  agg2x_k<<<dim3(128), dim3(GT), 0, stream>>>(ls2, ld2, h1pth, h1ptl, h1,
+                                              M2h, M2l);
+  h2_k<<<dim3(128), dim3(GT), 0, stream>>>(M2h, M2l, W2th, W2tl, b2,
+                                           h2s, h2h, h2l);
+  fc_k<<<dim3(32), dim3(GT), 0, stream>>>(h2h, h2l, fwth, fwtl, fcb, out);
+}
```

Result: no change. 140.3 us (-1.1%).
